# Optimization experiments

Hardware: AMD Instinct MI355X
Metric: run time of the kernel (lower is better)

Reference implementation:

```python
import jax, jax.numpy as jnp
import numpy as np
from jax import lax

# Fixed-point scales (powers of two, as in linger's luna/venus pipeline).
# scale_gi = input_scale * weight_ih_scale, scale_gh = hidden_scale * weight_hh_scale.
SCALE_GI = 2.0 ** 14
SCALE_GH = 2.0 ** 14
Q27 = 2.0 ** 27
Q15 = 2.0 ** 15
Q31 = 2.0 ** 31
INT32_MIN = -(2.0 ** 31)
INT32_MAX = 2.0 ** 31 - 1


def quant_round(x, scale):
    # QuantMode.floor_add: floor(x*scale + 0.5)/scale, with straight-through gradient
    # (linger QAT rounding uses STE).
    q = jnp.floor(x * scale + 0.5) / scale
    return x + lax.stop_gradient(q - x)


@jax.custom_vjp
def qsigmoid(x):
    # Quantize input to Q27 int32, evaluate sigmoid, output Q31 -> requant to Q15.
    i_q27 = jnp.clip(jnp.floor(x * Q27 + 0.5), INT32_MIN, INT32_MAX)
    s = jax.nn.sigmoid(i_q27 / Q27)
    out_q31 = jnp.floor(s * Q31 + 0.5)
    out_q15 = jnp.floor(out_q31 * (2.0 ** -16) + 0.5)  # luna_requant(31 -> 15)
    return out_q15 / Q15

def _qsig_fwd(x):
    return qsigmoid(x), x

def _qsig_bwd(x, g):
    s = jax.nn.sigmoid(x)
    return (g * s * (1.0 - s),)

qsigmoid.defvjp(_qsig_fwd, _qsig_bwd)


@jax.custom_vjp
def qtanh(x):
    i_q27 = jnp.clip(jnp.floor(x * Q27 + 0.5), INT32_MIN, INT32_MAX)
    t = jnp.tanh(i_q27 / Q27)
    out_q31 = jnp.floor(t * Q31 + 0.5)
    out_q15 = jnp.floor(out_q31 * (2.0 ** -16) + 0.5)
    return out_q15 / Q15

def _qtanh_fwd(x):
    return qtanh(x), x

def _qtanh_bwd(x, g):
    t = jnp.tanh(x)
    return (g * (1.0 - t * t),)

qtanh.defvjp(_qtanh_fwd, _qtanh_bwd)


def setup_inputs() -> dict:
    key = jax.random.key(0)
    k = jax.random.split(key, 6)
    B, I, H = 8192, 512, 512
    return {
        "input_x": jax.random.normal(k[0], (B, I), dtype=jnp.float32),
        "hidden": jax.random.normal(k[1], (B, H), dtype=jnp.float32),
        "weight_ih": jax.random.normal(k[2], (3 * H, I), dtype=jnp.float32) * 0.05,
        "weight_hh": jax.random.normal(k[3], (3 * H, H), dtype=jnp.float32) * 0.05,
        "bias_ih": jax.random.normal(k[4], (3 * H,), dtype=jnp.float32) * 0.05,
        "bias_hh": jax.random.normal(k[5], (3 * H,), dtype=jnp.float32) * 0.05,
    }


def reference(input_x, hidden, weight_ih, weight_hh, bias_ih, bias_hh):
    # Dense gate projections: [B, 3H]
    gi = input_x @ weight_ih.T + bias_ih
    gh = hidden @ weight_hh.T + bias_hh
    # Requant gate pre-activations to fixed-point grid (biasih/biashh quantizers)
    gi = quant_round(gi, SCALE_GI)
    gh = quant_round(gh, SCALE_GH)
    i_r, i_i, i_n = jnp.split(gi, 3, axis=1)
    h_r, h_i, h_n = jnp.split(gh, 3, axis=1)
    resetgate = qsigmoid(i_r + h_r)
    inputgate = qsigmoid(i_i + h_i)
    # h_n requantized to Q27, reset*h_n product requantized to Q15
    h_n = quant_round(h_n, Q27)
    resetgate_h_n = quant_round(resetgate * h_n, Q15)
    newgate = qtanh(resetgate_h_n + i_n)
    new_hidden = quant_round(hidden, Q15)
    hy = newgate + inputgate * (new_hidden - newgate)
    return hy
```

## Files before the change

### kernel.cpp

```cpp
#include <hip/hip_runtime.h>
#include <math.h>


typedef _Float16 f16x8  __attribute__((ext_vector_type(8)));
typedef _Float16 f16x4  __attribute__((ext_vector_type(4)));
typedef __bf16   bf16x8 __attribute__((ext_vector_type(8)));
typedef float    f32x16 __attribute__((ext_vector_type(16)));

namespace {

constexpr int Bsz = 8192, Ksz = 512, Hsz = 512;
constexpr int BM = 64, BN = 64;

constexpr unsigned WCH0    = 16384u;
constexpr unsigned NCHUNK  = 16384u + 3072u;
constexpr unsigned WS_F16  = NCHUNK * 512u;
constexpr size_t   WS_NEED = (size_t)WS_F16 * 2;

__device__ __forceinline__ float qround(float x, float s, float invs) {
    return floorf(x * s + 0.5f) * invs;
}

__device__ __forceinline__ float qsigmoid_dev(float x) {
    float iq = floorf(x * 134217728.0f + 0.5f);
    iq = fminf(fmaxf(iq, -2147483648.0f), 2147483648.0f);
    float e = __expf(-iq * 7.450580596923828125e-9f);
    float s = __builtin_amdgcn_rcpf(1.0f + e);
    float q31 = floorf(s * 2147483648.0f + 0.5f);
    float q15 = floorf(q31 * 1.52587890625e-5f + 0.5f);
    return q15 * 3.0517578125e-5f;
}

__device__ __forceinline__ float qtanh_dev(float x) {
    float iq = floorf(x * 134217728.0f + 0.5f);
    iq = fminf(fmaxf(iq, -2147483648.0f), 2147483648.0f);
    float z = iq * 7.450580596923828125e-9f;
    float e = __expf(2.0f * z);
    float t = 1.0f - 2.0f * __builtin_amdgcn_rcpf(e + 1.0f);
    float q31 = floorf(t * 2147483648.0f + 0.5f);
    float q15 = floorf(q31 * 1.52587890625e-5f + 0.5f);
    return q15 * 3.0517578125e-5f;
}

__device__ __forceinline__ void dma16(const void* g, void* l) {
    __builtin_amdgcn_global_load_lds(
        (const __attribute__((address_space(1))) unsigned int*)g,
        (__attribute__((address_space(3))) unsigned int*)l, 16, 0, 0);
}

__device__ __forceinline__ void split2(float a, float b, unsigned& hi, unsigned& lo) {
    unsigned ua = __float_as_uint(a); ua += 0x7fffu + ((ua >> 16) & 1u);
    unsigned ub = __float_as_uint(b); ub += 0x7fffu + ((ub >> 16) & 1u);
    hi = (ua >> 16) | (ub & 0xffff0000u);
    float ra = a - __uint_as_float(ua & 0xffff0000u);
    float rb = b - __uint_as_float(ub & 0xffff0000u);
    unsigned va = __float_as_uint(ra); va += 0x7fffu + ((va >> 16) & 1u);
    unsigned vb = __float_as_uint(rb); vb += 0x7fffu + ((vb >> 16) & 1u);
    lo = (va >> 16) | (vb & 0xffff0000u);
}

}

__global__ __launch_bounds__(256) void cvt_lds_f16(
    const float* __restrict__ x, const float* __restrict__ h,
    const float* __restrict__ wih, const float* __restrict__ whh,
    _Float16* __restrict__ ws)
{
    __shared__ __align__(16) _Float16 lt[8192];

    const int b2  = blockIdx.x;
    const int b   = b2 >> 1;
    const int kha = b2 & 1;
    const int tid = threadIdx.x;

    const float* src;
    unsigned chbase;
    if (b < 512) {
        const int arr = b >> 8, M32 = b & 255;
        src = (arr ? h : x) + (size_t)M32 * 32u * 512u;
        chbase = (unsigned)arr * 8192u + (unsigned)M32 * 32u;
    } else {
        const int w = b - 512;
        const int g = w >> 4, N32 = w & 15;
        const int rowLocal = (g % 3) * 512 + N32 * 32;
        src = (g < 3 ? wih : whh) + (size_t)rowLocal * 512u;
        chbase = WCH0 + (unsigned)((g * 16 + N32) * 32);
    }
    src += kha * 256;

#pragma unroll
    for (int rep = 0; rep < 8; ++rep) {
        const int idx = rep * 256 + tid;
        const int row = idx >> 6;
        const int q   = idx & 63;
        const float4 v = *(const float4*)(src + (size_t)row * 512 + q * 4);
        const int K16l = q >> 2;
        const int kh   = (q >> 1) & 1;
        const int half = (q & 1) * 4;
        const int rsw  = (row + (q >> 1)) & 31;
        f16x4 o;
        o[0] = (_Float16)v.x; o[1] = (_Float16)v.y;
        o[2] = (_Float16)v.z; o[3] = (_Float16)v.w;
        *(f16x4*)&lt[K16l * 512 + kh * 256 + rsw * 8 + half] = o;
    }
    __syncthreads();

    const int wid = tid >> 6, lane = tid & 63;
    const int kh  = lane >> 5, row = lane & 31;
#pragma unroll
    for (int cc = 0; cc < 4; ++cc) {
        const int K16l = wid * 4 + cc;
        const int rsw  = (row + 2 * K16l + kh) & 31;
        const f16x8 o = *(const f16x8*)&lt[K16l * 512 + kh * 256 + rsw * 8];
        *(f16x8*)(ws + (size_t)(chbase + (unsigned)(kha * 16 + K16l)) * 512u
                      + lane * 8) = o;
    }
}

__global__ __launch_bounds__(256, 2) void qgru_f16_dma3(
    const _Float16* __restrict__ ws, const float* __restrict__ hid,
    const float* __restrict__ bih, const float* __restrict__ bhh,
    float* __restrict__ out)
{
    __shared__ __align__(16) _Float16 lds[40960];

    const int t = threadIdx.x, lane = t & 63, wid = t >> 6;
    const int mt = wid >> 1, nt = wid & 1;

    const int bid = blockIdx.x;
    const int xcd = bid & 7, j = bid >> 3;
    const int xw  = xcd + 8 * (j & 7);
    const int yw  = j >> 3;
    const int m0  = xw * 128, n0 = yw * 64;

    unsigned goff[10];
    int      ldst[10];
#pragma unroll
    for (int c = 0; c < 10; ++c) {
        const int gi = wid * 10 + c;
        unsigned ch; int lo;
        if (gi < 16) {
            const int arr = gi >> 3, m32 = (gi >> 1) & 3, ks2 = gi & 1;
            ch = (unsigned)arr * 8192u
               + (unsigned)((m0 >> 5) + m32) * 32u + (unsigned)ks2;
            lo = ((arr * 4 + m32) * 2 + ks2) * 512;
        } else {
            const int bb = gi - 16;
            const int g = bb >> 2, n32 = (bb >> 1) & 1, ks2 = bb & 1;
            ch = WCH0 + (unsigned)((g * 16 + (n0 >> 5) + n32) * 32) + (unsigned)ks2;
            lo = 8192 + ((g * 2 + n32) * 2 + ks2) * 512;
        }
        goff[c] = ch * 1024u + (unsigned)lane * 16u;
        ldst[c] = lo;
    }

    f32x16 acc[4][2];
#pragma unroll
    for (int cid = 0; cid < 4; ++cid)
#pragma unroll
        for (int mf = 0; mf < 2; ++mf)
#pragma unroll
            for (int i = 0; i < 16; ++i) acc[cid][mf][i] = 0.0f;

    const char* wsb = (const char*)ws;
    const int lr = lane & 31, lk8 = (lane >> 5) * 8;

#pragma unroll
    for (int c = 0; c < 10; ++c)
        dma16(wsb + goff[c], &lds[ldst[c]]);

    for (int step = 0; step < 16; ++step) {
        const int cb = (step & 1) * 20480;

        if (step < 15) {
            const unsigned kb = (unsigned)(step + 1) * 2048u;
            const int nb = ((step + 1) & 1) * 20480;
#pragma unroll
            for (int c = 0; c < 10; ++c)
                dma16(wsb + goff[c] + kb, &lds[nb + ldst[c]]);
            asm volatile("s_waitcnt vmcnt(10)" ::: "memory");
        } else {
            asm volatile("s_waitcnt vmcnt(0)" ::: "memory");
        }
        __builtin_amdgcn_s_barrier();
        asm volatile("" ::: "memory");
        __builtin_amdgcn_s_setprio(1);

#pragma unroll
        for (int ks2 = 0; ks2 < 2; ++ks2) {
            const int lfo = cb + ks2 * 512 + lk8 * 32 + lr * 8;
            const f16x8 ax0 = *(const f16x8*)&lds[lfo + (mt * 2 + 0) * 1024];
            const f16x8 ax1 = *(const f16x8*)&lds[lfo + (mt * 2 + 1) * 1024];
            const f16x8 ah0 = *(const f16x8*)&lds[lfo + (4 + mt * 2 + 0) * 1024];
            const f16x8 ah1 = *(const f16x8*)&lds[lfo + (4 + mt * 2 + 1) * 1024];
#pragma unroll
            for (int g = 0; g < 6; ++g) {
                const f16x8 bv = *(const f16x8*)&lds[lfo + 8192 + (g * 2 + nt) * 1024];
                const int cid = (g < 3) ? g : (g == 5 ? 3 : g - 3);
                const f16x8 a0 = (g < 3) ? ax0 : ah0;
                const f16x8 a1 = (g < 3) ? ax1 : ah1;
                acc[cid][0] = __builtin_amdgcn_mfma_f32_32x32x16_f16(
                                  a0, bv, acc[cid][0], 0, 0, 0);
                acc[cid][1] = __builtin_amdgcn_mfma_f32_32x32x16_f16(
                                  a1, bv, acc[cid][1], 0, 0, 0);
            }
        }

        __builtin_amdgcn_s_setprio(0);
        asm volatile("" ::: "memory");
        __builtin_amdgcn_s_barrier();
    }

    constexpr float S14 = 16384.0f,     I14 = 1.0f / 16384.0f;
    constexpr float S15 = 32768.0f,     I15 = 1.0f / 32768.0f;

    const int lh = lane >> 5, l32 = lane & 31;
    const int n = n0 + nt * 32 + l32;
    const float brc = bih[n] + bhh[n];
    const float bic = bih[n + 512] + bhh[n + 512];
    const float bnn = bih[n + 1024];
    const float cnn = bhh[n + 1024];

#pragma unroll
    for (int mf = 0; mf < 2; ++mf) {
#pragma unroll
        for (int r = 0; r < 16; ++r) {
            const int row = (r & 3) + 8 * (r >> 2) + 4 * lh;
            const int m   = m0 + mt * 64 + mf * 32 + row;
            const float hv = hid[(size_t)m * Hsz + n];
            const float rg  = qsigmoid_dev(qround(acc[0][mf][r] + brc, S14, I14));
            const float ig  = qsigmoid_dev(qround(acc[1][mf][r] + bic, S14, I14));
            const float gin = qround(acc[2][mf][r] + bnn, S14, I14);
            const float ghn = qround(acc[3][mf][r] + cnn, S14, I14);
            const float rh  = qround(rg * ghn, S15, I15);
            const float ng  = qtanh_dev(rh + gin);
            const float nh  = qround(hv, S15, I15);
            out[(size_t)m * Hsz + n] = ng + ig * (nh - ng);
        }
    }
}

__global__ __launch_bounds__(256, 2) void qgru_mfma_bf16x3(
    const float* __restrict__ x, const float* __restrict__ hid,
    const float* __restrict__ wih, const float* __restrict__ whh,
    const float* __restrict__ bih, const float* __restrict__ bhh,
    float* __restrict__ out)
{
    __shared__ __align__(16) unsigned short lds[16384];

    const int t = threadIdx.x, lane = t & 63, wid = t >> 6;
    const int mt = wid >> 1, nt = wid & 1;
    const int m0 = blockIdx.x * BM, n0 = blockIdx.y * BN;
    const int s_r = t >> 2, s_k = (t & 3) << 2;
    const int s_kh = s_k >> 3, s_j = s_k & 7, s_rt = s_r >> 5, s_r32 = s_r & 31;

    const float* gA[2];
    gA[0] = x   + (size_t)(m0 + s_r) * Ksz + s_k;
    gA[1] = hid + (size_t)(m0 + s_r) * Ksz + s_k;
    const float* gW[6];
#pragma unroll
    for (int g = 0; g < 3; ++g) {
        gW[g]     = wih + (size_t)(g * Hsz + n0 + s_r) * Ksz + s_k;
        gW[g + 3] = whh + (size_t)(g * Hsz + n0 + s_r) * Ksz + s_k;
    }
    const int lh = lane >> 5, l32 = lane & 31;

    f32x16 acc[6];
#pragma unroll
    for (int g = 0; g < 6; ++g)
#pragma unroll
        for (int i = 0; i < 16; ++i) acc[g][i] = 0.0f;

    float4 vA[2], vW[6];
#pragma unroll
    for (int tt = 0; tt < 2; ++tt) vA[tt] = *(const float4*)gA[tt];
#pragma unroll
    for (int g = 0; g < 6; ++g)    vW[g]  = *(const float4*)gW[g];

    for (int k0 = 0; k0 < Ksz; k0 += 16) {
        __syncthreads();
#pragma unroll
        for (int tt = 0; tt < 2; ++tt) {
            unsigned h0, h1, l0, l1;
            split2(vA[tt].x, vA[tt].y, h0, l0);
            split2(vA[tt].z, vA[tt].w, h1, l1);
            unsigned bH = ((((tt*2+0)*2+s_rt)*2+s_kh)*32+s_r32)*8 + s_j;
            unsigned bL = ((((tt*2+1)*2+s_rt)*2+s_kh)*32+s_r32)*8 + s_j;
            *reinterpret_cast<uint2*>(&lds[bH]) = make_uint2(h0, h1);
            *reinterpret_cast<uint2*>(&lds[bL]) = make_uint2(l0, l1);
        }
#pragma unroll
        for (int g = 0; g < 6; ++g) {
            unsigned h0, h1, l0, l1;
            split2(vW[g].x, vW[g].y, h0, l0);
            split2(vW[g].z, vW[g].w, h1, l1);
            unsigned bH = 4096u + ((((g*2+0)*2+s_rt)*2+s_kh)*32+s_r32)*8 + s_j;
            unsigned bL = 4096u + ((((g*2+1)*2+s_rt)*2+s_kh)*32+s_r32)*8 + s_j;
            *reinterpret_cast<uint2*>(&lds[bH]) = make_uint2(h0, h1);
            *reinterpret_cast<uint2*>(&lds[bL]) = make_uint2(l0, l1);
        }
        __syncthreads();
        const int kn = (k0 + 16 < Ksz) ? (k0 + 16) : 0;
#pragma unroll
        for (int tt = 0; tt < 2; ++tt) vA[tt] = *(const float4*)(gA[tt] + kn);
#pragma unroll
        for (int g = 0; g < 6; ++g)    vW[g]  = *(const float4*)(gW[g] + kn);

        const bf16x8 ax_hi = *reinterpret_cast<const bf16x8*>(&lds[((((0)*2+mt)*2+lh)*32+l32)*8]);
        const bf16x8 ax_lo = *reinterpret_cast<const bf16x8*>(&lds[((((1)*2+mt)*2+lh)*32+l32)*8]);
        const bf16x8 ah_hi = *reinterpret_cast<const bf16x8*>(&lds[((((2)*2+mt)*2+lh)*32+l32)*8]);
        const bf16x8 ah_lo = *reinterpret_cast<const bf16x8*>(&lds[((((3)*2+mt)*2+lh)*32+l32)*8]);
#pragma unroll
        for (int g = 0; g < 6; ++g) {
            const bf16x8 b_hi = *reinterpret_cast<const bf16x8*>(&lds[4096u + ((((g*2+0)*2+nt)*2+lh)*32+l32)*8]);
            const bf16x8 b_lo = *reinterpret_cast<const bf16x8*>(&lds[4096u + ((((g*2+1)*2+nt)*2+lh)*32+l32)*8]);
            const bf16x8 a_hi = (g < 3) ? ax_hi : ah_hi;
            const bf16x8 a_lo = (g < 3) ? ax_lo : ah_lo;
            acc[g] = __builtin_amdgcn_mfma_f32_32x32x16_bf16(a_hi, b_hi, acc[g], 0, 0, 0);
            acc[g] = __builtin_amdgcn_mfma_f32_32x32x16_bf16(a_hi, b_lo, acc[g], 0, 0, 0);
            acc[g] = __builtin_amdgcn_mfma_f32_32x32x16_bf16(a_lo, b_hi, acc[g], 0, 0, 0);
        }
    }

    constexpr float S14 = 16384.0f,     I14 = 1.0f / 16384.0f;
    constexpr float S15 = 32768.0f,     I15 = 1.0f / 32768.0f;
    constexpr float S27 = 134217728.0f, I27 = 1.0f / 134217728.0f;
    const int n = n0 + nt * 32 + l32;
    const float br = bih[n], bi = bih[n + 512], bn = bih[n + 1024];
    const float cr = bhh[n], ci = bhh[n + 512], cn = bhh[n + 1024];
#pragma unroll
    for (int r = 0; r < 16; ++r) {
        const int row = (r & 3) + 8 * (r >> 2) + 4 * lh;
        const int m   = m0 + mt * 32 + row;
        const float hv = hid[(size_t)m * Hsz + n];
        float gir = qround(acc[0][r] + br, S14, I14);
        float gii = qround(acc[1][r] + bi, S14, I14);
        float gin = qround(acc[2][r] + bn, S14, I14);
        float ghr = qround(acc[3][r] + cr, S14, I14);
        float ghi = qround(acc[4][r] + ci, S14, I14);
        float ghn = qround(acc[5][r] + cn, S14, I14);
        float resetg = qsigmoid_dev(gir + ghr);
        float inputg = qsigmoid_dev(gii + ghi);
        float hn  = qround(ghn, S27, I27);
        float rh  = qround(resetg * hn, S15, I15);
        float newg = qtanh_dev(rh + gin);
        float nh  = qround(hv, S15, I15);
        out[(size_t)m * Hsz + n] = newg + inputg * (nh - newg);
    }
}

extern "C" void kernel_launch(void* const* d_in, const int* in_sizes, int n_in,
                              void* d_out, int out_size, void* d_ws, size_t ws_size,
                              hipStream_t stream) {
    const float* x   = (const float*)d_in[0];
    const float* hid = (const float*)d_in[1];
    const float* wih = (const float*)d_in[2];
    const float* whh = (const float*)d_in[3];
    const float* bih = (const float*)d_in[4];
    const float* bhh = (const float*)d_in[5];
    float* out = (float*)d_out;

    if (ws_size >= WS_NEED) {
        cvt_lds_f16<<<1216, 256, 0, stream>>>(
            x, hid, wih, whh, (_Float16*)d_ws);
        qgru_f16_dma3<<<512, 256, 0, stream>>>(
            (const _Float16*)d_ws, hid, bih, bhh, out);
    } else {
        dim3 grid(Bsz / BM, Hsz / BN);
        qgru_mfma_bf16x3<<<grid, dim3(256), 0, stream>>>(
            x, hid, wih, whh, bih, bhh, out);
    }
}
```

Before: 126.2 us.

## Load A fragments directly into registers, stage only weights through LDS

The A operand (x and hidden tiles) is now loaded straight from global memory into registers, double-buffered across two register sets, instead of going through LDS via DMA. Only the weight tiles still stream through LDS, which shrinks the LDS footprint from 80KB to 48KB per block and removes the A-side LDS reads. This trades more vector registers and redundant global reads of A (two waves share each A fragment) for less LDS traffic and possibly better occupancy.

```diff
diff --git a/kernel.cpp b/kernel.cpp
--- a/kernel.cpp
+++ b/kernel.cpp
@@ -117,12 +117,12 @@
     }
 }
 
-__global__ __launch_bounds__(256, 2) void qgru_f16_dma3(
+__global__ __launch_bounds__(256, 2) void qgru_f16_dma4(
     const _Float16* __restrict__ ws, const float* __restrict__ hid,
     const float* __restrict__ bih, const float* __restrict__ bhh,
     float* __restrict__ out)
 {
-    __shared__ __align__(16) _Float16 lds[40960];
+    __shared__ __align__(16) _Float16 lds[24576];
 
     const int t = threadIdx.x, lane = t & 63, wid = t >> 6;
     const int mt = wid >> 1, nt = wid & 1;
@@ -133,25 +133,25 @@
     const int yw  = j >> 3;
     const int m0  = xw * 128, n0 = yw * 64;
 
-    unsigned goff[10];
-    int      ldst[10];
-#pragma unroll
-    for (int c = 0; c < 10; ++c) {
-        const int gi = wid * 10 + c;
-        unsigned ch; int lo;
-        if (gi < 16) {
-            const int arr = gi >> 3, m32 = (gi >> 1) & 3, ks2 = gi & 1;
-            ch = (unsigned)arr * 8192u
-               + (unsigned)((m0 >> 5) + m32) * 32u + (unsigned)ks2;
-            lo = ((arr * 4 + m32) * 2 + ks2) * 512;
-        } else {
-            const int bb = gi - 16;
-            const int g = bb >> 2, n32 = (bb >> 1) & 1, ks2 = bb & 1;
-            ch = WCH0 + (unsigned)((g * 16 + (n0 >> 5) + n32) * 32) + (unsigned)ks2;
-            lo = 8192 + ((g * 2 + n32) * 2 + ks2) * 512;
-        }
-        goff[c] = ch * 1024u + (unsigned)lane * 16u;
-        ldst[c] = lo;
+    unsigned goffW[6];
+    int      ldstW[6];
+#pragma unroll
+    for (int c = 0; c < 6; ++c) {
+        const int gi = wid * 6 + c;
+        const int g = gi >> 2, n32 = (gi >> 1) & 1, ks2 = gi & 1;
+        const unsigned ch = WCH0
+            + (unsigned)((g * 16 + (n0 >> 5) + n32) * 32) + (unsigned)ks2;
+        goffW[c] = ch * 1024u + (unsigned)lane * 16u;
+        ldstW[c] = ((g * 2 + n32) * 2 + ks2) * 512;
+    }
+
+    unsigned offA[8];
+#pragma unroll
+    for (int i = 0; i < 8; ++i) {
+        const int ks2 = i >> 2, arr = (i >> 1) & 1, mf = i & 1;
+        const unsigned ch = (unsigned)arr * 8192u
+            + (unsigned)((m0 >> 5) + mt * 2 + mf) * 32u + (unsigned)ks2;
+        offA[i] = ch * 1024u + (unsigned)lane * 16u;
     }
 
     f32x16 acc[4][2];
@@ -165,51 +165,71 @@
     const char* wsb = (const char*)ws;
     const int lr = lane & 31, lk8 = (lane >> 5) * 8;
 
-#pragma unroll
-    for (int c = 0; c < 10; ++c)
-        dma16(wsb + goff[c], &lds[ldst[c]]);
-
-    for (int step = 0; step < 16; ++step) {
-        const int cb = (step & 1) * 20480;
-
-        if (step < 15) {
-            const unsigned kb = (unsigned)(step + 1) * 2048u;
-            const int nb = ((step + 1) & 1) * 20480;
-#pragma unroll
-            for (int c = 0; c < 10; ++c)
-                dma16(wsb + goff[c] + kb, &lds[nb + ldst[c]]);
-            asm volatile("s_waitcnt vmcnt(10)" ::: "memory");
-        } else {
-            asm volatile("s_waitcnt vmcnt(0)" ::: "memory");
-        }
-        __builtin_amdgcn_s_barrier();
-        asm volatile("" ::: "memory");
-        __builtin_amdgcn_s_setprio(1);
-
-#pragma unroll
-        for (int ks2 = 0; ks2 < 2; ++ks2) {
-            const int lfo = cb + ks2 * 512 + lk8 * 32 + lr * 8;
-            const f16x8 ax0 = *(const f16x8*)&lds[lfo + (mt * 2 + 0) * 1024];
-            const f16x8 ax1 = *(const f16x8*)&lds[lfo + (mt * 2 + 1) * 1024];
-            const f16x8 ah0 = *(const f16x8*)&lds[lfo + (4 + mt * 2 + 0) * 1024];
-            const f16x8 ah1 = *(const f16x8*)&lds[lfo + (4 + mt * 2 + 1) * 1024];
-#pragma unroll
-            for (int g = 0; g < 6; ++g) {
-                const f16x8 bv = *(const f16x8*)&lds[lfo + 8192 + (g * 2 + nt) * 1024];
-                const int cid = (g < 3) ? g : (g == 5 ? 3 : g - 3);
-                const f16x8 a0 = (g < 3) ? ax0 : ah0;
-                const f16x8 a1 = (g < 3) ? ax1 : ah1;
-                acc[cid][0] = __builtin_amdgcn_mfma_f32_32x32x16_f16(
-                                  a0, bv, acc[cid][0], 0, 0, 0);
-                acc[cid][1] = __builtin_amdgcn_mfma_f32_32x32x16_f16(
-                                  a1, bv, acc[cid][1], 0, 0, 0);
+    f16x8 aA[8], aB[8];
+
+#pragma unroll
+    for (int i = 0; i < 8; ++i)
+        aA[i] = *(const f16x8*)(wsb + offA[i]);
+#pragma unroll
+    for (int c = 0; c < 6; ++c)
+        dma16(wsb + goffW[c], &lds[ldstW[c]]);
+
+#define STEP_MFMA(ACUR, SLAB)                                                  \
+    _Pragma("unroll")                                                          \
+    for (int ks2 = 0; ks2 < 2; ++ks2) {                                        \
+        const int lfo = (SLAB) + ks2 * 512 + lk8 * 32 + lr * 8;                \
+        _Pragma("unroll")                                                      \
+        for (int g = 0; g < 6; ++g) {                                          \
+            const f16x8 bv = *(const f16x8*)&lds[lfo + (g * 2 + nt) * 1024];   \
+            const int cid = (g < 3) ? g : (g == 5 ? 3 : g - 3);                \
+            const f16x8 a0 = (g < 3) ? ACUR[ks2 * 4 + 0] : ACUR[ks2 * 4 + 2];  \
+            const f16x8 a1 = (g < 3) ? ACUR[ks2 * 4 + 1] : ACUR[ks2 * 4 + 3];  \
+            acc[cid][0] = __builtin_amdgcn_mfma_f32_32x32x16_f16(              \
+                              a0, bv, acc[cid][0], 0, 0, 0);                   \
+            acc[cid][1] = __builtin_amdgcn_mfma_f32_32x32x16_f16(              \
+                              a1, bv, acc[cid][1], 0, 0, 0);                   \
+        }                                                                      \
+    }
+
+    for (int sp = 0; sp < 8; ++sp) {
+        {
+            const unsigned kb = (unsigned)(2 * sp + 1) * 2048u;
+#pragma unroll
+            for (int i = 0; i < 8; ++i)
+                aB[i] = *(const f16x8*)(wsb + offA[i] + kb);
+#pragma unroll
+            for (int c = 0; c < 6; ++c)
+                dma16(wsb + goffW[c] + kb, &lds[12288 + ldstW[c]]);
+            asm volatile("s_waitcnt vmcnt(14)" ::: "memory");
+            __builtin_amdgcn_s_barrier();
+            __builtin_amdgcn_s_setprio(1);
+            STEP_MFMA(aA, 0)
+            __builtin_amdgcn_s_setprio(0);
+            asm volatile("" ::: "memory");
+            __builtin_amdgcn_s_barrier();
+        }
+        {
+            if (sp < 7) {
+                const unsigned kb = (unsigned)(2 * sp + 2) * 2048u;
+#pragma unroll
+                for (int i = 0; i < 8; ++i)
+                    aA[i] = *(const f16x8*)(wsb + offA[i] + kb);
+#pragma unroll
+                for (int c = 0; c < 6; ++c)
+                    dma16(wsb + goffW[c] + kb, &lds[ldstW[c]]);
+                asm volatile("s_waitcnt vmcnt(14)" ::: "memory");
+            } else {
+                asm volatile("s_waitcnt vmcnt(0)" ::: "memory");
             }
-        }
-
-        __builtin_amdgcn_s_setprio(0);
-        asm volatile("" ::: "memory");
-        __builtin_amdgcn_s_barrier();
-    }
+            __builtin_amdgcn_s_barrier();
+            __builtin_amdgcn_s_setprio(1);
+            STEP_MFMA(aB, 12288)
+            __builtin_amdgcn_s_setprio(0);
+            asm volatile("" ::: "memory");
+            __builtin_amdgcn_s_barrier();
+        }
+    }
+#undef STEP_MFMA
 
     constexpr float S14 = 16384.0f,     I14 = 1.0f / 16384.0f;
     constexpr float S15 = 32768.0f,     I15 = 1.0f / 32768.0f;
@@ -363,7 +383,7 @@
     if (ws_size >= WS_NEED) {
         cvt_lds_f16<<<1216, 256, 0, stream>>>(
             x, hid, wih, whh, (_Float16*)d_ws);
-        qgru_f16_dma3<<<512, 256, 0, stream>>>(
+        qgru_f16_dma4<<<512, 256, 0, stream>>>(
             (const _Float16*)d_ws, hid, bih, bhh, out);
     } else {
         dim3 grid(Bsz / BM, Hsz / BN);
```

Measured after the change: 129.0 us. +2.2%, slower.
